# Kernel optimization log

Measured on AMD Instinct MI355X. Metric: run time of the kernel, lower is better.

The kernel has to match this reference:

```python
import jax, jax.numpy as jnp
import numpy as np

H = 3072; NH = 24; HD = 128; MLP_D = 12288
B = 1; IMG = 1536; REF = 512; TXT = 256

def _gelu_tanh(x):
    return jax.nn.gelu(x, approximate=True)

def _ln(x, eps=1e-6):
    m = jnp.mean(x, axis=-1, keepdims=True)
    v = jnp.var(x, axis=-1, keepdims=True)
    return (x - m) * jax.lax.rsqrt(v + eps)

def _rms(x, g, eps=1e-6):
    return x * jax.lax.rsqrt(jnp.mean(x * x, axis=-1, keepdims=True) + eps) * g

def _rot_half(x):
    # interleaved rotate-half: (x0,x1,x2,x3,...) -> (-x1,x0,-x3,x2,...)
    x2 = x.reshape(x.shape[:-1] + (-1, 2))
    return jnp.stack([-x2[..., 1], x2[..., 0]], axis=-1).reshape(x.shape)

def setup_inputs():
    key = jax.random.key(0)
    ks = jax.random.split(key, 16)
    s = 0.02
    # rope tables for image tokens (interleaved layout, values repeated x2)
    inv_freq = 1.0 / (10000.0 ** (jnp.arange(0, HD // 2, dtype=jnp.float32) / (HD // 2)))
    ang = jnp.arange(IMG, dtype=jnp.float32)[:, None] * inv_freq[None, :]   # [IMG, HD//2]
    ang = jnp.repeat(ang, 2, axis=-1)                                       # [IMG, HD]
    return {
        'x':   jax.random.normal(ks[0], (B, IMG + TXT, H), jnp.float32),
        'vec': jax.random.normal(ks[1], (B, H), jnp.float32),
        'ref': jax.random.normal(ks[2], (B, REF, H), jnp.float32),
        'cos': jnp.cos(ang), 'sin': jnp.sin(ang),
        'mod_w':  jax.random.normal(ks[3], (H, 3 * H), jnp.float32) * s,
        'mod_b':  jnp.zeros((3 * H,), jnp.float32),
        'rf1_w':  jax.random.normal(ks[4], (H, H), jnp.float32) * s,
        'rf1_b':  jnp.zeros((H,), jnp.float32),
        'rf2_w':  jax.random.normal(ks[5], (H, H), jnp.float32) * s,
        'rf2_b':  jnp.zeros((H,), jnp.float32),
        'rln_g':  jnp.ones((H,), jnp.float32),
        'rln_b':  jnp.zeros((H,), jnp.float32),
        'lin1_w': jax.random.normal(ks[6], (H, 3 * H + MLP_D), jnp.float32) * s,
        'lin1_b': jnp.zeros((3 * H + MLP_D,), jnp.float32),
        'q_g':    jnp.ones((HD,), jnp.float32),
        'k_g':    jnp.ones((HD,), jnp.float32),
        'lin2_w': jax.random.normal(ks[7], (H + MLP_D, H), jnp.float32) * s,
        'lin2_b': jnp.zeros((H,), jnp.float32),
        'text_mask': jnp.ones((B, TXT), jnp.int32),
        'img_len': IMG, 'txt_len': TXT,
    }

def _forward(x, vec, ref, cos, sin, mod_w, mod_b, rf1_w, rf1_b, rf2_w, rf2_b,
             rln_g, rln_b, lin1_w, lin1_b, q_g, k_g, lin2_w, lin2_b,
             text_mask, img_len, txt_len):
    Bb = x.shape[0]
    ref_len = ref.shape[1]
    # modulation (ModulateDiT: SiLU -> Linear -> chunk(3))
    mod = jnp.dot(jax.nn.silu(vec), mod_w) + mod_b
    shift, scale, gate = jnp.split(mod, 3, axis=-1)
    x_mod = _ln(x) * (1.0 + scale[:, None]) + shift[:, None]
    # ref MLP + affine LayerNorm
    r = jnp.dot(_gelu_tanh(jnp.dot(ref, rf1_w) + rf1_b), rf2_w) + rf2_b
    r = _ln(r) * rln_g + rln_b
    # token reassembly: [img | ref | txt]
    xc = jnp.concatenate([x_mod[:, :img_len], r, x_mod[:, img_len:]], axis=1)
    h = jnp.dot(xc, lin1_w) + lin1_b
    qkv, mlp = h[..., :3 * H], h[..., 3 * H:]
    L2 = xc.shape[1]
    q, k, v = [t.reshape(Bb, L2, NH, HD) for t in jnp.split(qkv, 3, axis=-1)]
    # q drops the ref span; ref contributes K/V only
    q = jnp.concatenate([q[:, :img_len], q[:, img_len + ref_len:]], axis=1)
    q = _rms(q, q_g)
    k = _rms(k, k_g)
    # rotary only on image tokens
    c = cos[None, :, None, :]; s = sin[None, :, None, :]
    img_q = q[:, :img_len] * c + _rot_half(q[:, :img_len]) * s
    img_k = k[:, :img_len] * c + _rot_half(k[:, :img_len]) * s
    q = jnp.concatenate([img_q, q[:, img_len:]], axis=1)          # [B, Lq, NH, HD]
    k = jnp.concatenate([img_k, k[:, img_len:]], axis=1)          # [B, Lkv, NH, HD]
    # varlen mask (cu_seqlens semantics): valid attends valid, pad attends pad
    tmask = text_mask.astype(bool)
    qv  = jnp.concatenate([jnp.ones((Bb, img_len), bool), tmask], axis=1)
    kvv = jnp.concatenate([jnp.ones((Bb, img_len + ref_len), bool), tmask], axis=1)
    allowed = (qv[:, None, :, None] == kvv[:, None, None, :])     # [B,1,Lq,Lkv]
    scores = jnp.einsum('bqhd,bkhd->bhqk', q, k) * (HD ** -0.5)
    scores = jnp.where(allowed, scores, jnp.asarray(-1e9, scores.dtype))
    p = jax.nn.softmax(scores, axis=-1)
    attn = jnp.einsum('bhqk,bkhd->bqhd', p, v).reshape(Bb, img_len + txt_len, H)
    mlp = jnp.concatenate([mlp[:, :img_len], mlp[:, img_len + ref_len:]], axis=1)
    out = jnp.dot(jnp.concatenate([attn, _gelu_tanh(mlp)], axis=-1), lin2_w) + lin2_b
    return x + out * gate[:, None]

def reference(x, vec, ref, cos, sin, mod_w, mod_b, rf1_w, rf1_b, rf2_w, rf2_b,
              rln_g, rln_b, lin1_w, lin1_b, q_g, k_g, lin2_w, lin2_b,
              text_mask, img_len, txt_len):
    return _forward(x, vec, ref, cos, sin, mod_w, mod_b, rf1_w, rf1_b, rf2_w, rf2_b,
                    rln_g, rln_b, lin1_w, lin1_b, q_g, k_g, lin2_w, lin2_b,
                    text_mask, img_len, txt_len)
```

## Files before the change

kernel.cpp:

```cpp
#include <hip/hip_runtime.h>
#include <cstdint>
#include <cstddef>

typedef unsigned short u16;
typedef unsigned int   u32;
typedef __bf16 bf16_t;
typedef bf16_t bf16x8 __attribute__((ext_vector_type(8)));
typedef float  f32x4  __attribute__((ext_vector_type(4)));
typedef u16    u16x4  __attribute__((ext_vector_type(4)));


__device__ __forceinline__ float b2f(u16 b){ u32 u=((u32)b)<<16; float f; __builtin_memcpy(&f,&u,4); return f; }
__device__ __forceinline__ u16 f2b(float f){ u32 u; __builtin_memcpy(&u,&f,4); u = u + 0x7fffu + ((u>>16)&1u); return (u16)(u>>16); }
__device__ __forceinline__ float gelu_f(float x){
  const float u2 = 1.5957691216057308f*(x + 0.044715f*x*x*x);
  return x/(1.f + __expf(-u2));
}

__device__ __forceinline__ void gload_lds16(const void* g, void* l){
  __builtin_amdgcn_global_load_lds((const __attribute__((address_space(1))) void*)g,
                                   (__attribute__((address_space(3))) void*)l, 16, 0, 0);
}

template<int NW, bool MX>
__device__ __forceinline__ float bred(float v, float* red){
  #pragma unroll
  for (int o=32;o;o>>=1){ float u=__shfl_down(v,o,64); v = MX? fmaxf(v,u) : v+u; }
  const int t = threadIdx.x;
  if ((t&63)==0) red[t>>6]=v;
  __syncthreads();
  float r = red[0];
  #pragma unroll
  for (int i=1;i<NW;i++) r = MX? fmaxf(r,red[i]) : r+red[i];
  __syncthreads();
  return r;
}

__device__ __forceinline__ void unpack8(uint4 u, float* f){
  f[0]=b2f((u16)(u.x&0xffffu)); f[1]=b2f((u16)(u.x>>16));
  f[2]=b2f((u16)(u.y&0xffffu)); f[3]=b2f((u16)(u.y>>16));
  f[4]=b2f((u16)(u.z&0xffffu)); f[5]=b2f((u16)(u.z>>16));
  f[6]=b2f((u16)(u.w&0xffffu)); f[7]=b2f((u16)(u.w>>16));
}
__device__ __forceinline__ uint4 pack8(const float* f){
  uint4 u;
  u.x = (u32)f2b(f[0]) | ((u32)f2b(f[1])<<16);
  u.y = (u32)f2b(f[2]) | ((u32)f2b(f[3])<<16);
  u.z = (u32)f2b(f[4]) | ((u32)f2b(f[5])<<16);
  u.w = (u32)f2b(f[6]) | ((u32)f2b(f[7])<<16);
  return u;
}

__global__ void modv_part(const float* __restrict__ vec, const float* __restrict__ W,
                          float* __restrict__ part){
  __shared__ float s[128];
  const int t = threadIdx.x;
  const int j = blockIdx.x*256 + t;
  const int i0 = blockIdx.y*128;
  if (t < 128){ float v = vec[i0+t]; s[t] = v/(1.f+__expf(-v)); }
  __syncthreads();
  float acc = 0.f;
  #pragma unroll 8
  for (int i=0;i<128;i++) acc += s[i]*W[(size_t)(i0+i)*9216 + j];
  part[(size_t)blockIdx.y*9216 + j] = acc;
}
__global__ void modv_reduce(const float* __restrict__ part, const float* __restrict__ mb,
                            float* __restrict__ modp){
  const int j = blockIdx.x*256 + threadIdx.x;
  float a = mb[j];
  #pragma unroll
  for (int c=0;c<24;c++) a += part[(size_t)c*9216 + j];
  modp[j] = a;
}

__global__ __launch_bounds__(256)
void convT(const float* __restrict__ W, u16* __restrict__ Wt, int Kd, int Nd){
  __shared__ float Ls[64][65];
  const int t = threadIdx.x;
  const int n0 = blockIdx.x*64, k0 = blockIdx.y*64;
  const int tr = t>>4;
  const int tc = (t&15)*4;
  #pragma unroll
  for (int p=0;p<4;p++){
    const int kk = tr + p*16;
    const float4 v = *(const float4*)(W + (size_t)(k0+kk)*Nd + n0 + tc);
    Ls[kk][tc+0]=v.x; Ls[kk][tc+1]=v.y; Ls[kk][tc+2]=v.z; Ls[kk][tc+3]=v.w;
  }
  __syncthreads();
  #pragma unroll
  for (int p=0;p<4;p++){
    const int nn = tr + p*16;
    u16x4 o;
    o.x = f2b(Ls[tc+0][nn]); o.y = f2b(Ls[tc+1][nn]);
    o.z = f2b(Ls[tc+2][nn]); o.w = f2b(Ls[tc+3][nn]);
    *(u16x4*)(Wt + (size_t)(n0+nn)*Kd + k0 + tc) = o;
  }
}

__global__ void convertF2B(const float* __restrict__ src, u16* __restrict__ dst){
  const size_t i = ((size_t)blockIdx.x*256 + threadIdx.x)*4;
  const float4 v = *(const float4*)(src+i);
  u16x4 o; o.x=f2b(v.x); o.y=f2b(v.y); o.z=f2b(v.z); o.w=f2b(v.w);
  *(u16x4*)(dst+i) = o;
}

__global__ void ln_modulate(const float* __restrict__ x, const float* __restrict__ modp,
                            u16* __restrict__ xc){
  __shared__ float red[4];
  const int row = blockIdx.x, t = threadIdx.x;
  const float* xr = x + (size_t)row*3072;
  float4 v[3]; float s=0.f, ss=0.f;
  #pragma unroll
  for (int k=0;k<3;k++){
    v[k] = *(const float4*)(xr + t*4 + k*1024);
    s  += v[k].x+v[k].y+v[k].z+v[k].w;
    ss += v[k].x*v[k].x+v[k].y*v[k].y+v[k].z*v[k].z+v[k].w*v[k].w;
  }
  s  = bred<4,false>(s, red);
  ss = bred<4,false>(ss, red);
  const float mean = s*(1.f/3072.f);
  const float inv = rsqrtf(ss*(1.f/3072.f)-mean*mean + 1e-6f);
  const int orow = row<1536 ? row : row+512;
  u16* o = xc + (size_t)orow*3072;
  const float* shiftp = modp; const float* scalep = modp+3072;
  #pragma unroll
  for (int k=0;k<3;k++){
    const int j = t*4 + k*1024;
    const float4 sc = *(const float4*)(scalep+j);
    const float4 sh = *(const float4*)(shiftp+j);
    u16x4 ov;
    ov.x = f2b((v[k].x-mean)*inv*(1.f+sc.x)+sh.x);
    ov.y = f2b((v[k].y-mean)*inv*(1.f+sc.y)+sh.y);
    ov.z = f2b((v[k].z-mean)*inv*(1.f+sc.z)+sh.z);
    ov.w = f2b((v[k].w-mean)*inv*(1.f+sc.w)+sh.w);
    *(u16x4*)(o+j) = ov;
  }
}

__global__ void ln_ref(const float* __restrict__ rt, const float* __restrict__ g,
                       const float* __restrict__ b, u16* __restrict__ xc){
  __shared__ float red[4];
  const int row = blockIdx.x, t = threadIdx.x;
  const float* xr = rt + (size_t)row*3072;
  float4 v[3]; float s=0.f, ss=0.f;
  #pragma unroll
  for (int k=0;k<3;k++){
    v[k] = *(const float4*)(xr + t*4 + k*1024);
    s  += v[k].x+v[k].y+v[k].z+v[k].w;
    ss += v[k].x*v[k].x+v[k].y*v[k].y+v[k].z*v[k].z+v[k].w*v[k].w;
  }
  s  = bred<4,false>(s, red);
  ss = bred<4,false>(ss, red);
  const float mean = s*(1.f/3072.f);
  const float inv = rsqrtf(ss*(1.f/3072.f)-mean*mean + 1e-6f);
  u16* o = xc + (size_t)(1536+row)*3072;
  #pragma unroll
  for (int k=0;k<3;k++){
    const int j = t*4 + k*1024;
    const float4 gv = *(const float4*)(g+j);
    const float4 bv = *(const float4*)(b+j);
    u16x4 ov;
    ov.x = f2b((v[k].x-mean)*inv*gv.x+bv.x);
    ov.y = f2b((v[k].y-mean)*inv*gv.y+bv.y);
    ov.z = f2b((v[k].z-mean)*inv*gv.z+bv.z);
    ov.w = f2b((v[k].w-mean)*inv*gv.w+bv.w);
    *(u16x4*)(o+j) = ov;
  }
}

__global__ void qk_prep(const u16* __restrict__ h, const float* __restrict__ qg,
                        const float* __restrict__ kg, const float* __restrict__ cosb,
                        const float* __restrict__ sinb, u16* __restrict__ Q,
                        u16* __restrict__ Kb){
  __shared__ float red[4];
  const int row = blockIdx.x, hd = blockIdx.y, d = threadIdx.x;
  const u16* hr = h + (size_t)row*21504;
  const float kv = b2f(hr[3072 + hd*128 + d]);
  const bool doq = (row < 1536) || (row >= 2048);
  const float qv = doq ? b2f(hr[hd*128 + d]) : 0.f;
  float a = kv*kv, b = qv*qv;
  #pragma unroll
  for (int o=32;o;o>>=1){ a += __shfl_down(a,o,64); b += __shfl_down(b,o,64); }
  if ((d&63)==0){ red[(d>>6)*2] = a; red[(d>>6)*2+1] = b; }
  __syncthreads();
  const float kinv = rsqrtf((red[0]+red[2])*(1.f/128.f) + 1e-6f);
  const float qinv = rsqrtf((red[1]+red[3])*(1.f/128.f) + 1e-6f);
  float kn = kv*kinv*kg[d];
  float qn = qv*qinv*qg[d];
  if (row < 1536){
    const float c  = cosb[row*128 + d];
    const float sn = sinb[row*128 + d];
    const float ko = b2f(hr[3072 + hd*128 + (d^1)])*kinv*kg[d^1];
    const float qo = b2f(hr[hd*128 + (d^1)])*qinv*qg[d^1];
    const float krh = (d&1) ? ko : -ko;
    const float qrh = (d&1) ? qo : -qo;
    kn = kn*c + krh*sn;
    qn = qn*c + qrh*sn;
  }
  Kb[((size_t)hd*2304 + row)*128 + d] = f2b(kn);
  if (doq){
    const int qrow = row<1536 ? row : row-512;
    Q[((size_t)hd*1792 + qrow)*128 + d] = f2b(qn);
  }
}

__global__ void v_transpose(const u16* __restrict__ h, u16* __restrict__ VT){
  __shared__ u16 Ls[32][33];
  const int tx = threadIdx.x, ty = threadIdx.y;
  const int l0 = blockIdx.x*32, d0 = blockIdx.y*32, hd = blockIdx.z;
  #pragma unroll
  for (int r=0;r<4;r++)
    Ls[ty+r*8][tx] = h[(size_t)(l0+ty+r*8)*21504 + 6144 + hd*128 + d0 + tx];
  __syncthreads();
  #pragma unroll
  for (int r=0;r<4;r++)
    VT[((size_t)hd*128 + d0+ty+r*8)*2304 + l0 + tx] = Ls[tx][ty+r*8];
}

__global__ void gelu_mlp(const u16* __restrict__ h, u16* __restrict__ out2){
  const int q = blockIdx.x;
  const int hrow = q<1536 ? q : q+512;
  const int j = blockIdx.y*2048 + threadIdx.x*8;
  const uint4 u = *(const uint4*)(h + (size_t)hrow*21504 + 9216 + j);
  float f[8]; unpack8(u, f);
  #pragma unroll
  for (int e=0;e<8;e++) f[e] = gelu_f(f[e]);
  const uint4 o = pack8(f);
  *(uint4*)(out2 + (size_t)q*15360 + 3072 + j) = o;
}

template<int EPI>
__global__ __launch_bounds__(256)
void gemm_bt(const u16* __restrict__ A, const u16* __restrict__ Bt,
             const float* __restrict__ bias, void* __restrict__ Cv,
             int K, int ldA, int ldB, int ldC,
             long long sA, long long sB, long long sC)
{
  __shared__ u16 As[128*32];
  __shared__ u16 Bs[128*32];
  const int t = threadIdx.x;
  const int w = t>>6, lane = t&63;
  const int bm = blockIdx.y, bn = blockIdx.x, bz = blockIdx.z;
  const u16* Ab = A + (size_t)((long long)bz*sA) + (size_t)bm*128*ldA;
  const u16* Bb = Bt + (size_t)((long long)bz*sB) + (size_t)bn*128*ldB;
  const int wm = w>>1, wn = w&1;
  const int lr = lane&15, lk = lane>>4;
  const int row0 = t>>2, kp0 = (t&3)*8;
  char* AsB = (char*)As; char* BsB = (char*)Bs;
  const int off0 = w*1024;
  const int off1 = 4096 + w*1024;
  f32x4 acc[4][4] = {};

  for (int kt = 0; kt < K; kt += 32){
    __syncthreads();
    gload_lds16(Ab + (size_t)row0*ldA + kt + kp0,      AsB + off0);
    gload_lds16(Ab + (size_t)(row0+64)*ldA + kt + kp0, AsB + off1);
    gload_lds16(Bb + (size_t)row0*ldB + kt + kp0,      BsB + off0);
    gload_lds16(Bb + (size_t)(row0+64)*ldB + kt + kp0, BsB + off1);
    __syncthreads();
    bf16x8 av[4], bv[4];
    #pragma unroll
    for (int i=0;i<4;i++) av[i] = *(const bf16x8*)(As + (wm*64+i*16+lr)*32 + lk*8);
    #pragma unroll
    for (int j=0;j<4;j++) bv[j] = *(const bf16x8*)(Bs + (wn*64+j*16+lr)*32 + lk*8);
    #pragma unroll
    for (int i=0;i<4;i++)
      #pragma unroll
      for (int j=0;j<4;j++)
        acc[i][j] = __builtin_amdgcn_mfma_f32_16x16x32_bf16(av[i], bv[j], acc[i][j], 0,0,0);
  }

  const int mBase = bm*128 + wm*64;
  const int nBase = bn*128 + wn*64;
  #pragma unroll
  for (int i=0;i<4;i++){
    #pragma unroll
    for (int j=0;j<4;j++){
      #pragma unroll
      for (int r=0;r<4;r++){
        const int m = mBase + i*16 + lk*4 + r;
        const int n = nBase + j*16 + lr;
        const float v = acc[i][j][r];
        const long long idx = (long long)bz*sC + (long long)m*ldC + n;
        if (EPI==6){
          ((float*)Cv)[idx] = v;
        } else {
          ((u16*)Cv)[idx] = f2b(v + bias[n]);
        }
      }
    }
  }
}

__global__ void comb_gelu(const float* __restrict__ P, const float* __restrict__ b,
                          u16* __restrict__ o){
  const size_t e = ((size_t)blockIdx.x*256 + threadIdx.x)*4;
  const int n = (int)(e % 3072);
  const size_t S = (size_t)512*3072;
  float4 a = *(const float4*)(P + e);
  #pragma unroll
  for (int c=1;c<6;c++){
    const float4 p = *(const float4*)(P + c*S + e);
    a.x+=p.x; a.y+=p.y; a.z+=p.z; a.w+=p.w;
  }
  const float4 bb = *(const float4*)(b + n);
  u16x4 ov;
  ov.x = f2b(gelu_f(a.x+bb.x)); ov.y = f2b(gelu_f(a.y+bb.y));
  ov.z = f2b(gelu_f(a.z+bb.z)); ov.w = f2b(gelu_f(a.w+bb.w));
  *(u16x4*)(o + e) = ov;
}
__global__ void comb_bias(const float* __restrict__ P, const float* __restrict__ b,
                          float* __restrict__ o){
  const size_t e = ((size_t)blockIdx.x*256 + threadIdx.x)*4;
  const int n = (int)(e % 3072);
  const size_t S = (size_t)512*3072;
  float4 a = *(const float4*)(P + e);
  #pragma unroll
  for (int c=1;c<6;c++){
    const float4 p = *(const float4*)(P + c*S + e);
    a.x+=p.x; a.y+=p.y; a.z+=p.z; a.w+=p.w;
  }
  const float4 bb = *(const float4*)(b + n);
  float4 ov; ov.x=a.x+bb.x; ov.y=a.y+bb.y; ov.z=a.z+bb.z; ov.w=a.w+bb.w;
  *(float4*)(o + e) = ov;
}

#define G256_BAR()  __builtin_amdgcn_s_barrier()
#define G256_LGKM() do{ asm volatile("s_waitcnt lgkmcnt(0)" ::: "memory"); \
                        __builtin_amdgcn_sched_barrier(0); }while(0)

template<int CEPI>
__global__ __launch_bounds__(512,2)
void gemm256(const u16* __restrict__ A, const u16* __restrict__ Bt,
             const float* __restrict__ bias, void* __restrict__ Cv,
             int Kc, int ld, int ldC, int nbn, int ntile, long long sC, int nwg, int gm)
{
  __shared__ char smem[131072];
  const int t = threadIdx.x;
  const int wid = t>>6, lane = t&63;
  const int lr = lane&15, lk = lane>>4;
  const int wm = wid>>2, wn = wid&3;

  const int orig = blockIdx.x;
  const int q8 = nwg>>3, r8 = nwg&7;
  const int xcd = orig&7, jj = orig>>3;
  const int wg = (xcd<r8 ? xcd*(q8+1) : r8*(q8+1) + (xcd-r8)*q8) + jj;
  int sk, bm, bn;
  if (gm > 0){
    const int band = wg / (gm*nbn);
    const int rr = wg - band*(gm*nbn);
    bn = rr / gm;
    bm = band*gm + (rr - bn*gm);
    sk = 0;
  } else {
    sk = wg / ntile;
    const int rem = wg - sk*ntile;
    bm = rem / nbn; bn = rem % nbn;
  }

  const u16* Agl = A  + (size_t)bm*256*ld + (size_t)sk*Kc;
  const u16* Bgl = Bt + (size_t)bn*256*ld + (size_t)sk*Kc;
  const int NT = Kc>>6;

  const int d0 = wid*64 + lane;
  const int sr = d0>>3;
  const size_t soff = (size_t)sr*ld + (size_t)(((d0&7)^(sr&7))<<3);

  const int xsl0 = ((lk    ) ^ (lr&7))<<4;
  const int xsl1 = ((lk | 4) ^ (lr&7))<<4;

  f32x4 acc[8][4] = {};
  bf16x8 bv[4][2];

  auto STAGE = [&](const u16* g, int h, int kt, char* ldsMat){
    const u16* s0 = g + (size_t)(h*128)*ld + kt + soff;
    char* l0 = ldsMat + h*16384 + wid*1024;
    gload_lds16(s0, l0);
    gload_lds16(s0 + (size_t)64*ld, l0 + 8192);
  };

  STAGE(Agl, 0, 0, smem);
  STAGE(Agl, 1, 0, smem);
  STAGE(Bgl, 0, 0, smem + 32768);
  STAGE(Bgl, 1, 0, smem + 32768);
  if (NT > 1){
    STAGE(Bgl, 0, 64, smem + 65536 + 32768);
    STAGE(Bgl, 1, 64, smem + 65536 + 32768);
    asm volatile("s_waitcnt vmcnt(4)" ::: "memory");
  } else {
    asm volatile("s_waitcnt vmcnt(0)" ::: "memory");
  }
  G256_BAR();

  for (int tt = 0; tt < NT; ++tt){
    char* cA = smem + (tt&1)*65536;
    char* cB = cA + 32768;
    char* nA = smem + ((tt+1)&1)*65536;
    const int kt1 = (tt+1)<<6, kt2 = (tt+2)<<6;
    const bool stA = (tt+1) < NT, stB = (tt+2) < NT;

    {
      const char* ab0 = cA + (wm*128 + 0*32 + lr)*128;
      const char* ab1 = cA + (wm*128 + 1*32 + lr)*128;
      bf16x8 a00 = *(const bf16x8*)(ab0 + xsl0);
      bf16x8 a01 = *(const bf16x8*)(ab0 + xsl1);
      bf16x8 a02 = *(const bf16x8*)(ab0 + 2048 + xsl0);
      bf16x8 a03 = *(const bf16x8*)(ab0 + 2048 + xsl1);
      bf16x8 a10 = *(const bf16x8*)(ab1 + xsl0);
      bf16x8 a11 = *(const bf16x8*)(ab1 + xsl1);
      bf16x8 a12 = *(const bf16x8*)(ab1 + 2048 + xsl0);
      bf16x8 a13 = *(const bf16x8*)(ab1 + 2048 + xsl1);
      #pragma unroll
      for (int j=0;j<4;j++){
        const char* bbase = cB + (wn*64 + j*16 + lr)*128;
        bv[j][0] = *(const bf16x8*)(bbase + xsl0);
        bv[j][1] = *(const bf16x8*)(bbase + xsl1);
      }
      if (stA){ STAGE(Agl, 0, kt1, nA); STAGE(Agl, 1, kt1, nA); }
      G256_BAR();
      G256_LGKM();
      __builtin_amdgcn_s_setprio(1);
      #pragma unroll
      for (int j=0;j<4;j++){
        acc[0][j] = __builtin_amdgcn_mfma_f32_16x16x32_bf16(a00, bv[j][0], acc[0][j], 0,0,0);
        acc[0][j] = __builtin_amdgcn_mfma_f32_16x16x32_bf16(a01, bv[j][1], acc[0][j], 0,0,0);
        acc[1][j] = __builtin_amdgcn_mfma_f32_16x16x32_bf16(a02, bv[j][0], acc[1][j], 0,0,0);
        acc[1][j] = __builtin_amdgcn_mfma_f32_16x16x32_bf16(a03, bv[j][1], acc[1][j], 0,0,0);
        acc[2][j] = __builtin_amdgcn_mfma_f32_16x16x32_bf16(a10, bv[j][0], acc[2][j], 0,0,0);
        acc[2][j] = __builtin_amdgcn_mfma_f32_16x16x32_bf16(a11, bv[j][1], acc[2][j], 0,0,0);
        acc[3][j] = __builtin_amdgcn_mfma_f32_16x16x32_bf16(a12, bv[j][0], acc[3][j], 0,0,0);
        acc[3][j] = __builtin_amdgcn_mfma_f32_16x16x32_bf16(a13, bv[j][1], acc[3][j], 0,0,0);
      }
      __builtin_amdgcn_s_setprio(0);
      G256_BAR();
    }
    {
      const char* ab2 = cA + (wm*128 + 2*32 + lr)*128;
      const char* ab3 = cA + (wm*128 + 3*32 + lr)*128;
      bf16x8 a20 = *(const bf16x8*)(ab2 + xsl0);
      bf16x8 a21 = *(const bf16x8*)(ab2 + xsl1);
      bf16x8 a22 = *(const bf16x8*)(ab2 + 2048 + xsl0);
      bf16x8 a23 = *(const bf16x8*)(ab2 + 2048 + xsl1);
      bf16x8 a30 = *(const bf16x8*)(ab3 + xsl0);
      bf16x8 a31 = *(const bf16x8*)(ab3 + xsl1);
      bf16x8 a32 = *(const bf16x8*)(ab3 + 2048 + xsl0);
      bf16x8 a33 = *(const bf16x8*)(ab3 + 2048 + xsl1);
      if (stB){ STAGE(Bgl, 0, kt2, cB); STAGE(Bgl, 1, kt2, cB); }
      G256_BAR();
      G256_LGKM();
      __builtin_amdgcn_s_setprio(1);
      #pragma unroll
      for (int j=0;j<4;j++){
        acc[4][j] = __builtin_amdgcn_mfma_f32_16x16x32_bf16(a20, bv[j][0], acc[4][j], 0,0,0);
        acc[4][j] = __builtin_amdgcn_mfma_f32_16x16x32_bf16(a21, bv[j][1], acc[4][j], 0,0,0);
        acc[5][j] = __builtin_amdgcn_mfma_f32_16x16x32_bf16(a22, bv[j][0], acc[5][j], 0,0,0);
        acc[5][j] = __builtin_amdgcn_mfma_f32_16x16x32_bf16(a23, bv[j][1], acc[5][j], 0,0,0);
        acc[6][j] = __builtin_amdgcn_mfma_f32_16x16x32_bf16(a30, bv[j][0], acc[6][j], 0,0,0);
        acc[6][j] = __builtin_amdgcn_mfma_f32_16x16x32_bf16(a31, bv[j][1], acc[6][j], 0,0,0);
        acc[7][j] = __builtin_amdgcn_mfma_f32_16x16x32_bf16(a32, bv[j][0], acc[7][j], 0,0,0);
        acc[7][j] = __builtin_amdgcn_mfma_f32_16x16x32_bf16(a33, bv[j][1], acc[7][j], 0,0,0);
      }
      __builtin_amdgcn_s_setprio(0);
      if (stB)      { asm volatile("s_waitcnt vmcnt(4)" ::: "memory"); }
      else if (stA) { asm volatile("s_waitcnt vmcnt(0)" ::: "memory"); }
      G256_BAR();
    }
  }

  const int mB = bm*256 + wm*128 + lk*4;
  const int nB = bn*256 + wn*64 + lr;
  #pragma unroll
  for (int fi=0; fi<8; fi++){
    #pragma unroll
    for (int j=0; j<4; j++){
      const int n = nB + j*16;
      const float bb = (CEPI==0) ? bias[n] : 0.f;
      #pragma unroll
      for (int r=0;r<4;r++){
        const int m = mB + fi*16 + r;
        if (CEPI==0){
          ((u16*)Cv)[(size_t)m*ldC + n] = f2b(acc[fi][j][r] + bb);
        } else {
          ((float*)Cv)[(size_t)sk*sC + (size_t)m*ldC + n] = acc[fi][j][r];
        }
      }
    }
  }
}

__global__ __launch_bounds__(512,4)
void flash_attn(const u16* __restrict__ Qb, const u16* __restrict__ Kb,
                const u16* __restrict__ VT, const int* __restrict__ tmask,
                u16* __restrict__ out2)
{
  __shared__ __attribute__((aligned(16))) char smf[81920];
  char* Ks0 = smf;
  char* Vs0 = smf + 32768;
  char* Ps  = smf + 65536;
  const int t = threadIdx.x, wid = t>>6, lane = t&63;
  const int lr = lane&15, hi = lane>>4;
  const int head = blockIdx.y, qt = blockIdx.x;
  const int q0 = qt*128;
  const u16* Qg = Qb + ((size_t)head*1792 + q0)*128;
  const u16* Kg = Kb + (size_t)head*2304*128;
  const u16* Vg = VT + (size_t)head*128*2304;
  const float SCALE = 0.08838834764831845f;

  u32 kbits = 0;
  #pragma unroll
  for (int i=0;i<16;i++) kbits |= (u32)(tmask[i*16 + lr] != 0) << i;
  int fqr[4];
  #pragma unroll
  for (int r=0;r<4;r++){
    const int q = q0 + wid*16 + hi*4 + r;
    fqr[r] = (q < 1536) ? 1 : (tmask[q-1536] != 0);
  }

  #pragma unroll
  for (int c=0;c<4;c++){
    const int s = c*512 + wid*64 + lane;
    const int row = s>>4, dsl = s&15;
    gload_lds16(Qg + (size_t)row*128 + ((dsl ^ (row&7))<<3),
                Vs0 + (size_t)(c*512 + wid*64)*16);
  }
  #pragma unroll
  for (int c=0;c<2;c++){
    const int s = c*512 + wid*64 + lane;
    const int row = s>>4, dsl = s&15;
    gload_lds16(Kg + (size_t)row*128 + ((dsl ^ (row&7))<<3),
                Ks0 + (size_t)(c*512 + wid*64)*16);
  }
  asm volatile("s_waitcnt vmcnt(0)" ::: "memory");
  __syncthreads();

  bf16x8 av[4];
  {
    const int row = wid*16 + lr;
    #pragma unroll
    for (int ks=0;ks<4;ks++)
      av[ks] = *(const bf16x8*)(Vs0 + row*256 + (((ks*4+hi) ^ (row&7))<<4));
  }
  asm volatile("s_waitcnt lgkmcnt(0)" ::: "memory");
  __builtin_amdgcn_sched_barrier(0);
  __syncthreads();

  #pragma unroll
  for (int c=0;c<2;c++){
    const int s = c*512 + wid*64 + lane;
    const int row = s>>3, dsl = s&7;
    gload_lds16(Vg + (size_t)row*2304 + ((dsl ^ (row&7))<<3),
                Vs0 + (size_t)(c*512 + wid*64)*16);
  }
  asm volatile("s_waitcnt vmcnt(0)" ::: "memory");
  __syncthreads();

  f32x4 acc[8] = {};
  float m_[4], l_[4];
  #pragma unroll
  for (int r=0;r<4;r++){ m_[r] = -3e38f; l_[r] = 0.f; }

  for (int kt = 0; kt < 36; ++kt){
    char* Kc = Ks0 + (kt&1)*16384;
    char* Vc = Vs0 + (kt&1)*16384;
    if (kt+1 < 36){
      char* Kn = Ks0 + ((kt+1)&1)*16384;
      char* Vn = Vs0 + ((kt+1)&1)*16384;
      #pragma unroll
      for (int c=0;c<2;c++){
        const int s = c*512 + wid*64 + lane;
        { const int row = s>>4, dsl = s&15;
          gload_lds16(Kg + (size_t)((kt+1)*64 + row)*128 + ((dsl ^ (row&7))<<3),
                      Kn + (size_t)(c*512 + wid*64)*16); }
        { const int row = s>>3, dsl = s&7;
          gload_lds16(Vg + (size_t)row*2304 + (kt+1)*64 + ((dsl ^ (row&7))<<3),
                      Vn + (size_t)(c*512 + wid*64)*16); }
      }
    }
    f32x4 sacc[4] = {};
    #pragma unroll
    for (int ks=0;ks<4;ks++){
      #pragma unroll
      for (int j=0;j<4;j++){
        const int row = j*16 + lr;
        bf16x8 bk = *(const bf16x8*)(Kc + row*256 + (((ks*4+hi) ^ (row&7))<<4));
        sacc[j] = __builtin_amdgcn_mfma_f32_16x16x32_bf16(av[ks], bk, sacc[j], 0,0,0);
      }
    }
    int gkj[4];
    #pragma unroll
    for (int j=0;j<4;j++)
      gkj[j] = (kt < 32) ? 1 : (int)((kbits >> ((kt-32)*4 + j)) & 1u);
    float p[4][4]; bool alw[4][4];
    float mt[4] = {-3e38f,-3e38f,-3e38f,-3e38f};
    #pragma unroll
    for (int j=0;j<4;j++){
      #pragma unroll
      for (int r=0;r<4;r++){
        const float s = sacc[j][r]*SCALE;
        const bool a = (fqr[r] == gkj[j]);
        alw[j][r] = a; p[j][r] = s;
        if (a) mt[r] = fmaxf(mt[r], s);
      }
    }
    #pragma unroll
    for (int r=0;r<4;r++){
      #pragma unroll
      for (int o=1;o<16;o<<=1) mt[r] = fmaxf(mt[r], __shfl_xor(mt[r], o, 64));
      const float nm = fmaxf(m_[r], mt[r]);
      const float cr = __expf(m_[r] - nm);
      m_[r] = nm;
      l_[r] *= cr;
      #pragma unroll
      for (int jp=0;jp<8;jp++) acc[jp][r] *= cr;
    }
    float rs[4] = {0.f,0.f,0.f,0.f};
    #pragma unroll
    for (int j=0;j<4;j++){
      #pragma unroll
      for (int r=0;r<4;r++){
        const float pv = alw[j][r] ? __expf(p[j][r] - m_[r]) : 0.f;
        p[j][r] = pv; rs[r] += pv;
      }
    }
    #pragma unroll
    for (int r=0;r<4;r++){
      #pragma unroll
      for (int o=1;o<16;o<<=1) rs[r] += __shfl_xor(rs[r], o, 64);
      l_[r] += rs[r];
    }
    #pragma unroll
    for (int j=0;j<4;j++){
      #pragma unroll
      for (int r=0;r<4;r++){
        const int q = wid*16 + hi*4 + r;
        const int k = j*16 + lr;
        *(u16*)(Ps + q*128 + (((k>>3) ^ (q&7))<<4) + (k&7)*2) = f2b(p[j][r]);
      }
    }
    asm volatile("s_waitcnt lgkmcnt(0)" ::: "memory");
    __builtin_amdgcn_sched_barrier(0);
    bf16x8 pa[2];
    {
      const int row = wid*16 + lr;
      #pragma unroll
      for (int ks2=0;ks2<2;ks2++)
        pa[ks2] = *(const bf16x8*)(Ps + row*128 + (((ks2*4+hi) ^ (row&7))<<4));
    }
    #pragma unroll
    for (int ks2=0;ks2<2;ks2++){
      #pragma unroll
      for (int jp=0;jp<8;jp++){
        const int row = jp*16 + lr;
        bf16x8 bvv = *(const bf16x8*)(Vc + row*128 + (((ks2*4+hi) ^ (row&7))<<4));
        acc[jp] = __builtin_amdgcn_mfma_f32_16x16x32_bf16(pa[ks2], bvv, acc[jp], 0,0,0);
      }
    }
    asm volatile("s_waitcnt vmcnt(0)" ::: "memory");
    __syncthreads();
  }

  float inv[4];
  #pragma unroll
  for (int r=0;r<4;r++) inv[r] = 1.f/l_[r];
  #pragma unroll
  for (int jp=0;jp<8;jp++){
    #pragma unroll
    for (int r=0;r<4;r++){
      const size_t q = q0 + wid*16 + hi*4 + r;
      out2[q*15360 + head*128 + jp*16 + lr] = f2b(acc[jp][r]*inv[r]);
    }
  }
}

__global__ void lin2_fin(const float* __restrict__ P, const float* __restrict__ x,
                         const float* __restrict__ bias, const float* __restrict__ gate,
                         float* __restrict__ out){
  const size_t e = ((size_t)blockIdx.x*256 + threadIdx.x)*4;
  const int n = (int)(e % 3072);
  const size_t S = (size_t)1792*3072;
  float4 a = *(const float4*)(P + e);
  #pragma unroll
  for (int c=1;c<6;c++){
    const float4 p = *(const float4*)(P + c*S + e);
    a.x+=p.x; a.y+=p.y; a.z+=p.z; a.w+=p.w;
  }
  const float4 bb = *(const float4*)(bias + n);
  const float4 gg = *(const float4*)(gate + n);
  const float4 xv = *(const float4*)(x + e);
  float4 o;
  o.x = xv.x + (a.x+bb.x)*gg.x;
  o.y = xv.y + (a.y+bb.y)*gg.y;
  o.z = xv.z + (a.z+bb.z)*gg.z;
  o.w = xv.w + (a.w+bb.w)*gg.w;
  *(float4*)(out + e) = o;
}

extern "C" void kernel_launch(void* const* d_in, const int* in_sizes, int n_in,
                              void* d_out, int out_size, void* d_ws, size_t ws_size,
                              hipStream_t stream)
{
  (void)in_sizes; (void)n_in; (void)out_size; (void)ws_size;
  const float* x     = (const float*)d_in[0];
  const float* vec   = (const float*)d_in[1];
  const float* ref   = (const float*)d_in[2];
  const float* cosb  = (const float*)d_in[3];
  const float* sinb  = (const float*)d_in[4];
  const float* mod_w = (const float*)d_in[5];
  const float* mod_b = (const float*)d_in[6];
  const float* rf1_w = (const float*)d_in[7];
  const float* rf1_b = (const float*)d_in[8];
  const float* rf2_w = (const float*)d_in[9];
  const float* rf2_b = (const float*)d_in[10];
  const float* rln_g = (const float*)d_in[11];
  const float* rln_b = (const float*)d_in[12];
  const float* lin1_w= (const float*)d_in[13];
  const float* lin1_b= (const float*)d_in[14];
  const float* q_g   = (const float*)d_in[15];
  const float* k_g   = (const float*)d_in[16];
  const float* lin2_w= (const float*)d_in[17];
  const float* lin2_b= (const float*)d_in[18];
  const int*   tmask = (const int*)d_in[19];
  float* out = (float*)d_out;
  char* ws = (char*)d_ws;

  float* modp = (float*)(ws + 0);
  float* part = (float*)(ws + 36864);
  u16*  w2t   = (u16*)(ws + 921600);
  u16*  Qb    = (u16*)(ws + 95293440ll);
  u16*  Kb    = (u16*)(ws + 106303488ll);
  u16*  VT    = (u16*)(ws + 120459264ll);
  u16*  out2  = (u16*)(ws + 134615040ll);
  u16*  w1t   = (u16*)(ws + 189665280ll);
  u16*  xc    = (u16*)(ws + 321785856ll);
  u16*  rf1t  = (u16*)(ws + 335941632ll);
  u16*  rf2t  = (u16*)(ws + 354816000ll);
  u16*  refb  = (u16*)(ws + 373690368ll);
  u16*  tb    = (u16*)(ws + 376836096ll);
  float* rtmp = (float*)(ws + 379981824ll);
  float* rp   = (float*)(ws + 386273280ll);
  u16*  hbuf  = (u16*)(ws + 335941632ll);
  float* p2b  = (float*)(ws + 189665280ll);

  modv_part<<<dim3(36,24),256,0,stream>>>(vec, mod_w, part);
  modv_reduce<<<36,256,0,stream>>>(part, mod_b, modp);
  convT<<<dim3(48,48),  256,0,stream>>>(rf1_w, rf1t, 3072, 3072);
  convT<<<dim3(48,48),  256,0,stream>>>(rf2_w, rf2t, 3072, 3072);
  convT<<<dim3(336,48), 256,0,stream>>>(lin1_w, w1t, 3072, 21504);
  convT<<<dim3(48,240), 256,0,stream>>>(lin2_w, w2t, 15360, 3072);
  convertF2B<<<1536,256,0,stream>>>(ref, refb);
  ln_modulate<<<1792,256,0,stream>>>(x, modp, xc);
  gemm_bt<6><<<dim3(24,4,6),256,0,stream>>>(refb, rf1t, nullptr, rp, 512, 3072,3072,3072,
                                            512,512, (long long)512*3072);
  comb_gelu<<<1536,256,0,stream>>>(rp, rf1_b, tb);
  gemm_bt<6><<<dim3(24,4,6),256,0,stream>>>(tb, rf2t, nullptr, rp, 512, 3072,3072,3072,
                                            512,512, (long long)512*3072);
  comb_bias<<<1536,256,0,stream>>>(rp, rf2_b, rtmp);
  ln_ref<<<512,256,0,stream>>>(rtmp, rln_g, rln_b, xc);
  gemm256<0><<<756,512,0,stream>>>(xc, w1t, lin1_b, hbuf, 3072, 3072, 21504, 84, 756, 0, 756, 3);
  gelu_mlp<<<dim3(1792,6),256,0,stream>>>(hbuf, out2);
  qk_prep<<<dim3(2304,24),128,0,stream>>>(hbuf, q_g, k_g, cosb, sinb, Qb, Kb);
  v_transpose<<<dim3(72,4,24),dim3(32,8),0,stream>>>(hbuf, VT);
  flash_attn<<<dim3(14,24),512,0,stream>>>(Qb, Kb, VT, tmask, out2);
  gemm256<1><<<504,512,0,stream>>>(out2, w2t, nullptr, p2b, 2560, 15360, 3072, 12, 84,
                                   (long long)1792*3072, 504, 0);
  lin2_fin<<<5376,256,0,stream>>>(p2b, x, lin2_b, modp + 6144, out);
}
```

Baseline: 906.6 us.

## Skip unused lin1 tiles for ref tokens and make the GEMM persistent

Result: no change. 905.7 us (-0.1%).

```diff
diff --git a/kernel.cpp b/kernel.cpp
--- a/kernel.cpp
+++ b/kernel.cpp
@@ -329,6 +329,18 @@
 #define G256_LGKM() do{ asm volatile("s_waitcnt lgkmcnt(0)" ::: "memory"); \
                         __builtin_amdgcn_sched_barrier(0); }while(0)
 
+__device__ __forceinline__ void lin1_map(int tw, int& bm, int& bn){
+  if (tw < 504){
+    const int band = tw/252; const int rr = tw - band*252;
+    bn = rr/3; bm = band*3 + (rr - bn*3);
+  } else if (tw < 588){
+    bm = 8; bn = tw - 504;
+  } else {
+    const int rem = tw - 588;
+    bm = 6 + (rem&1); bn = 12 + (rem>>1);
+  }
+}
+
 template<int CEPI>
 __global__ __launch_bounds__(512,2)
 void gemm256(const u16* __restrict__ A, const u16* __restrict__ Bt,
@@ -341,150 +353,160 @@
   const int lr = lane&15, lk = lane>>4;
   const int wm = wid>>2, wn = wid&3;
 
-  const int orig = blockIdx.x;
-  const int q8 = nwg>>3, r8 = nwg&7;
-  const int xcd = orig&7, jj = orig>>3;
-  const int wg = (xcd<r8 ? xcd*(q8+1) : r8*(q8+1) + (xcd-r8)*q8) + jj;
-  int sk, bm, bn;
-  if (gm > 0){
-    const int band = wg / (gm*nbn);
-    const int rr = wg - band*(gm*nbn);
-    bn = rr / gm;
-    bm = band*gm + (rr - bn*gm);
-    sk = 0;
+  int niter = 1;
+  int bmA[2], bnA[2], skA[2];
+  if (gm == -1){
+    const int b = blockIdx.x;
+    lin1_map(b, bmA[0], bnA[0]); skA[0] = 0;
+    if (b + 512 < 636){ lin1_map(b + 512, bmA[1], bnA[1]); skA[1] = 0; niter = 2; }
   } else {
-    sk = wg / ntile;
-    const int rem = wg - sk*ntile;
-    bm = rem / nbn; bn = rem % nbn;
-  }
-
-  const u16* Agl = A  + (size_t)bm*256*ld + (size_t)sk*Kc;
-  const u16* Bgl = Bt + (size_t)bn*256*ld + (size_t)sk*Kc;
+    const int orig = blockIdx.x;
+    const int q8 = nwg>>3, r8 = nwg&7;
+    const int xcd = orig&7, jj = orig>>3;
+    const int wg = (xcd<r8 ? xcd*(q8+1) : r8*(q8+1) + (xcd-r8)*q8) + jj;
+    if (gm > 0){
+      const int band = wg / (gm*nbn);
+      const int rr = wg - band*(gm*nbn);
+      bnA[0] = rr / gm;
+      bmA[0] = band*gm + (rr - bnA[0]*gm);
+      skA[0] = 0;
+    } else {
+      skA[0] = wg / ntile;
+      const int rem = wg - skA[0]*ntile;
+      bmA[0] = rem / nbn; bnA[0] = rem % nbn;
+    }
+  }
+
   const int NT = Kc>>6;
-
   const int d0 = wid*64 + lane;
   const int sr = d0>>3;
   const size_t soff = (size_t)sr*ld + (size_t)(((d0&7)^(sr&7))<<3);
-
   const int xsl0 = ((lk    ) ^ (lr&7))<<4;
   const int xsl1 = ((lk | 4) ^ (lr&7))<<4;
 
-  f32x4 acc[8][4] = {};
-  bf16x8 bv[4][2];
-
-  auto STAGE = [&](const u16* g, int h, int kt, char* ldsMat){
-    const u16* s0 = g + (size_t)(h*128)*ld + kt + soff;
-    char* l0 = ldsMat + h*16384 + wid*1024;
-    gload_lds16(s0, l0);
-    gload_lds16(s0 + (size_t)64*ld, l0 + 8192);
-  };
-
-  STAGE(Agl, 0, 0, smem);
-  STAGE(Agl, 1, 0, smem);
-  STAGE(Bgl, 0, 0, smem + 32768);
-  STAGE(Bgl, 1, 0, smem + 32768);
-  if (NT > 1){
-    STAGE(Bgl, 0, 64, smem + 65536 + 32768);
-    STAGE(Bgl, 1, 64, smem + 65536 + 32768);
-    asm volatile("s_waitcnt vmcnt(4)" ::: "memory");
-  } else {
-    asm volatile("s_waitcnt vmcnt(0)" ::: "memory");
-  }
-  G256_BAR();
-
-  for (int tt = 0; tt < NT; ++tt){
-    char* cA = smem + (tt&1)*65536;
-    char* cB = cA + 32768;
-    char* nA = smem + ((tt+1)&1)*65536;
-    const int kt1 = (tt+1)<<6, kt2 = (tt+2)<<6;
-    const bool stA = (tt+1) < NT, stB = (tt+2) < NT;
-
-    {
-      const char* ab0 = cA + (wm*128 + 0*32 + lr)*128;
-      const char* ab1 = cA + (wm*128 + 1*32 + lr)*128;
-      bf16x8 a00 = *(const bf16x8*)(ab0 + xsl0);
-      bf16x8 a01 = *(const bf16x8*)(ab0 + xsl1);
-      bf16x8 a02 = *(const bf16x8*)(ab0 + 2048 + xsl0);
-      bf16x8 a03 = *(const bf16x8*)(ab0 + 2048 + xsl1);
-      bf16x8 a10 = *(const bf16x8*)(ab1 + xsl0);
-      bf16x8 a11 = *(const bf16x8*)(ab1 + xsl1);
-      bf16x8 a12 = *(const bf16x8*)(ab1 + 2048 + xsl0);
-      bf16x8 a13 = *(const bf16x8*)(ab1 + 2048 + xsl1);
-      #pragma unroll
-      for (int j=0;j<4;j++){
-        const char* bbase = cB + (wn*64 + j*16 + lr)*128;
-        bv[j][0] = *(const bf16x8*)(bbase + xsl0);
-        bv[j][1] = *(const bf16x8*)(bbase + xsl1);
-      }
-      if (stA){ STAGE(Agl, 0, kt1, nA); STAGE(Agl, 1, kt1, nA); }
-      G256_BAR();
-      G256_LGKM();
-      __builtin_amdgcn_s_setprio(1);
-      #pragma unroll
-      for (int j=0;j<4;j++){
-        acc[0][j] = __builtin_amdgcn_mfma_f32_16x16x32_bf16(a00, bv[j][0], acc[0][j], 0,0,0);
-        acc[0][j] = __builtin_amdgcn_mfma_f32_16x16x32_bf16(a01, bv[j][1], acc[0][j], 0,0,0);
-        acc[1][j] = __builtin_amdgcn_mfma_f32_16x16x32_bf16(a02, bv[j][0], acc[1][j], 0,0,0);
-        acc[1][j] = __builtin_amdgcn_mfma_f32_16x16x32_bf16(a03, bv[j][1], acc[1][j], 0,0,0);
-        acc[2][j] = __builtin_amdgcn_mfma_f32_16x16x32_bf16(a10, bv[j][0], acc[2][j], 0,0,0);
-        acc[2][j] = __builtin_amdgcn_mfma_f32_16x16x32_bf16(a11, bv[j][1], acc[2][j], 0,0,0);
-        acc[3][j] = __builtin_amdgcn_mfma_f32_16x16x32_bf16(a12, bv[j][0], acc[3][j], 0,0,0);
-        acc[3][j] = __builtin_amdgcn_mfma_f32_16x16x32_bf16(a13, bv[j][1], acc[3][j], 0,0,0);
-      }
-      __builtin_amdgcn_s_setprio(0);
-      G256_BAR();
-    }
-    {
-      const char* ab2 = cA + (wm*128 + 2*32 + lr)*128;
-      const char* ab3 = cA + (wm*128 + 3*32 + lr)*128;
-      bf16x8 a20 = *(const bf16x8*)(ab2 + xsl0);
-      bf16x8 a21 = *(const bf16x8*)(ab2 + xsl1);
-      bf16x8 a22 = *(const bf16x8*)(ab2 + 2048 + xsl0);
-      bf16x8 a23 = *(const bf16x8*)(ab2 + 2048 + xsl1);
-      bf16x8 a30 = *(const bf16x8*)(ab3 + xsl0);
-      bf16x8 a31 = *(const bf16x8*)(ab3 + xsl1);
-      bf16x8 a32 = *(const bf16x8*)(ab3 + 2048 + xsl0);
-      bf16x8 a33 = *(const bf16x8*)(ab3 + 2048 + xsl1);
-      if (stB){ STAGE(Bgl, 0, kt2, cB); STAGE(Bgl, 1, kt2, cB); }
-      G256_BAR();
-      G256_LGKM();
-      __builtin_amdgcn_s_setprio(1);
-      #pragma unroll
-      for (int j=0;j<4;j++){
-        acc[4][j] = __builtin_amdgcn_mfma_f32_16x16x32_bf16(a20, bv[j][0], acc[4][j], 0,0,0);
-        acc[4][j] = __builtin_amdgcn_mfma_f32_16x16x32_bf16(a21, bv[j][1], acc[4][j], 0,0,0);
-        acc[5][j] = __builtin_amdgcn_mfma_f32_16x16x32_bf16(a22, bv[j][0], acc[5][j], 0,0,0);
-        acc[5][j] = __builtin_amdgcn_mfma_f32_16x16x32_bf16(a23, bv[j][1], acc[5][j], 0,0,0);
-        acc[6][j] = __builtin_amdgcn_mfma_f32_16x16x32_bf16(a30, bv[j][0], acc[6][j], 0,0,0);
-        acc[6][j] = __builtin_amdgcn_mfma_f32_16x16x32_bf16(a31, bv[j][1], acc[6][j], 0,0,0);
-        acc[7][j] = __builtin_amdgcn_mfma_f32_16x16x32_bf16(a32, bv[j][0], acc[7][j], 0,0,0);
-        acc[7][j] = __builtin_amdgcn_mfma_f32_16x16x32_bf16(a33, bv[j][1], acc[7][j], 0,0,0);
-      }
-      __builtin_amdgcn_s_setprio(0);
-      if (stB)      { asm volatile("s_waitcnt vmcnt(4)" ::: "memory"); }
-      else if (stA) { asm volatile("s_waitcnt vmcnt(0)" ::: "memory"); }
-      G256_BAR();
-    }
-  }
-
-  const int mB = bm*256 + wm*128 + lk*4;
-  const int nB = bn*256 + wn*64 + lr;
-  #pragma unroll
-  for (int fi=0; fi<8; fi++){
-    #pragma unroll
-    for (int j=0; j<4; j++){
-      const int n = nB + j*16;
-      const float bb = (CEPI==0) ? bias[n] : 0.f;
-      #pragma unroll
-      for (int r=0;r<4;r++){
-        const int m = mB + fi*16 + r;
-        if (CEPI==0){
-          ((u16*)Cv)[(size_t)m*ldC + n] = f2b(acc[fi][j][r] + bb);
-        } else {
-          ((float*)Cv)[(size_t)sk*sC + (size_t)m*ldC + n] = acc[fi][j][r];
+  for (int it = 0; it < niter; ++it){
+    const int bm = bmA[it], bn = bnA[it], sk = skA[it];
+    const u16* Agl = A  + (size_t)bm*256*ld + (size_t)sk*Kc;
+    const u16* Bgl = Bt + (size_t)bn*256*ld + (size_t)sk*Kc;
+
+    f32x4 acc[8][4] = {};
+    bf16x8 bv[4][2];
+
+    auto STAGE = [&](const u16* g, int h, int kt, char* ldsMat){
+      const u16* s0 = g + (size_t)(h*128)*ld + kt + soff;
+      char* l0 = ldsMat + h*16384 + wid*1024;
+      gload_lds16(s0, l0);
+      gload_lds16(s0 + (size_t)64*ld, l0 + 8192);
+    };
+
+    STAGE(Agl, 0, 0, smem);
+    STAGE(Agl, 1, 0, smem);
+    STAGE(Bgl, 0, 0, smem + 32768);
+    STAGE(Bgl, 1, 0, smem + 32768);
+    if (NT > 1){
+      STAGE(Bgl, 0, 64, smem + 65536 + 32768);
+      STAGE(Bgl, 1, 64, smem + 65536 + 32768);
+      asm volatile("s_waitcnt vmcnt(4)" ::: "memory");
+    } else {
+      asm volatile("s_waitcnt vmcnt(0)" ::: "memory");
+    }
+    G256_BAR();
+
+    for (int tt = 0; tt < NT; ++tt){
+      char* cA = smem + (tt&1)*65536;
+      char* cB = cA + 32768;
+      char* nA = smem + ((tt+1)&1)*65536;
+      const int kt1 = (tt+1)<<6, kt2 = (tt+2)<<6;
+      const bool stA = (tt+1) < NT, stB = (tt+2) < NT;
+
+      {
+        const char* ab0 = cA + (wm*128 + 0*32 + lr)*128;
+        const char* ab1 = cA + (wm*128 + 1*32 + lr)*128;
+        bf16x8 a00 = *(const bf16x8*)(ab0 + xsl0);
+        bf16x8 a01 = *(const bf16x8*)(ab0 + xsl1);
+        bf16x8 a02 = *(const bf16x8*)(ab0 + 2048 + xsl0);
+        bf16x8 a03 = *(const bf16x8*)(ab0 + 2048 + xsl1);
+        bf16x8 a10 = *(const bf16x8*)(ab1 + xsl0);
+        bf16x8 a11 = *(const bf16x8*)(ab1 + xsl1);
+        bf16x8 a12 = *(const bf16x8*)(ab1 + 2048 + xsl0);
+        bf16x8 a13 = *(const bf16x8*)(ab1 + 2048 + xsl1);
+        #pragma unroll
+        for (int j=0;j<4;j++){
+          const char* bbase = cB + (wn*64 + j*16 + lr)*128;
+          bv[j][0] = *(const bf16x8*)(bbase + xsl0);
+          bv[j][1] = *(const bf16x8*)(bbase + xsl1);
         }
-      }
-    }
+        if (stA){ STAGE(Agl, 0, kt1, nA); STAGE(Agl, 1, kt1, nA); }
+        G256_BAR();
+        G256_LGKM();
+        __builtin_amdgcn_s_setprio(1);
+        #pragma unroll
+        for (int j=0;j<4;j++){
+          acc[0][j] = __builtin_amdgcn_mfma_f32_16x16x32_bf16(a00, bv[j][0], acc[0][j], 0,0,0);
+          acc[0][j] = __builtin_amdgcn_mfma_f32_16x16x32_bf16(a01, bv[j][1], acc[0][j], 0,0,0);
+          acc[1][j] = __builtin_amdgcn_mfma_f32_16x16x32_bf16(a02, bv[j][0], acc[1][j], 0,0,0);
+          acc[1][j] = __builtin_amdgcn_mfma_f32_16x16x32_bf16(a03, bv[j][1], acc[1][j], 0,0,0);
+          acc[2][j] = __builtin_amdgcn_mfma_f32_16x16x32_bf16(a10, bv[j][0], acc[2][j], 0,0,0);
+          acc[2][j] = __builtin_amdgcn_mfma_f32_16x16x32_bf16(a11, bv[j][1], acc[2][j], 0,0,0);
+          acc[3][j] = __builtin_amdgcn_mfma_f32_16x16x32_bf16(a12, bv[j][0], acc[3][j], 0,0,0);
+          acc[3][j] = __builtin_amdgcn_mfma_f32_16x16x32_bf16(a13, bv[j][1], acc[3][j], 0,0,0);
+        }
+        __builtin_amdgcn_s_setprio(0);
+        G256_BAR();
+      }
+      {
+        const char* ab2 = cA + (wm*128 + 2*32 + lr)*128;
+        const char* ab3 = cA + (wm*128 + 3*32 + lr)*128;
+        bf16x8 a20 = *(const bf16x8*)(ab2 + xsl0);
+        bf16x8 a21 = *(const bf16x8*)(ab2 + xsl1);
+        bf16x8 a22 = *(const bf16x8*)(ab2 + 2048 + xsl0);
+        bf16x8 a23 = *(const bf16x8*)(ab2 + 2048 + xsl1);
+        bf16x8 a30 = *(const bf16x8*)(ab3 + xsl0);
+        bf16x8 a31 = *(const bf16x8*)(ab3 + xsl1);
+        bf16x8 a32 = *(const bf16x8*)(ab3 + 2048 + xsl0);
+        bf16x8 a33 = *(const bf16x8*)(ab3 + 2048 + xsl1);
+        if (stB){ STAGE(Bgl, 0, kt2, cB); STAGE(Bgl, 1, kt2, cB); }
+        G256_BAR();
+        G256_LGKM();
+        __builtin_amdgcn_s_setprio(1);
+        #pragma unroll
+        for (int j=0;j<4;j++){
+          acc[4][j] = __builtin_amdgcn_mfma_f32_16x16x32_bf16(a20, bv[j][0], acc[4][j], 0,0,0);
+          acc[4][j] = __builtin_amdgcn_mfma_f32_16x16x32_bf16(a21, bv[j][1], acc[4][j], 0,0,0);
+          acc[5][j] = __builtin_amdgcn_mfma_f32_16x16x32_bf16(a22, bv[j][0], acc[5][j], 0,0,0);
+          acc[5][j] = __builtin_amdgcn_mfma_f32_16x16x32_bf16(a23, bv[j][1], acc[5][j], 0,0,0);
+          acc[6][j] = __builtin_amdgcn_mfma_f32_16x16x32_bf16(a30, bv[j][0], acc[6][j], 0,0,0);
+          acc[6][j] = __builtin_amdgcn_mfma_f32_16x16x32_bf16(a31, bv[j][1], acc[6][j], 0,0,0);
+          acc[7][j] = __builtin_amdgcn_mfma_f32_16x16x32_bf16(a32, bv[j][0], acc[7][j], 0,0,0);
+          acc[7][j] = __builtin_amdgcn_mfma_f32_16x16x32_bf16(a33, bv[j][1], acc[7][j], 0,0,0);
+        }
+        __builtin_amdgcn_s_setprio(0);
+        if (stB)      { asm volatile("s_waitcnt vmcnt(4)" ::: "memory"); }
+        else if (stA) { asm volatile("s_waitcnt vmcnt(0)" ::: "memory"); }
+        G256_BAR();
+      }
+    }
+
+    const int mB = bm*256 + wm*128 + lk*4;
+    const int nB = bn*256 + wn*64 + lr;
+    #pragma unroll
+    for (int fi=0; fi<8; fi++){
+      #pragma unroll
+      for (int j=0; j<4; j++){
+        const int n = nB + j*16;
+        const float bb = (CEPI==0) ? bias[n] : 0.f;
+        #pragma unroll
+        for (int r=0;r<4;r++){
+          const int m = mB + fi*16 + r;
+          if (CEPI==0){
+            ((u16*)Cv)[(size_t)m*ldC + n] = f2b(acc[fi][j][r] + bb);
+          } else {
+            ((float*)Cv)[(size_t)sk*sC + (size_t)m*ldC + n] = acc[fi][j][r];
+          }
+        }
+      }
+    }
+    if (it+1 < niter) __syncthreads();
   }
 }
 
@@ -756,7 +778,7 @@
                                             512,512, (long long)512*3072);
   comb_bias<<<1536,256,0,stream>>>(rp, rf2_b, rtmp);
   ln_ref<<<512,256,0,stream>>>(rtmp, rln_g, rln_b, xc);
-  gemm256<0><<<756,512,0,stream>>>(xc, w1t, lin1_b, hbuf, 3072, 3072, 21504, 84, 756, 0, 756, 3);
+  gemm256<0><<<512,512,0,stream>>>(xc, w1t, lin1_b, hbuf, 3072, 3072, 21504, 84, 636, 0, 512, -1);
   gelu_mlp<<<dim3(1792,6),256,0,stream>>>(hbuf, out2);
   qk_prep<<<dim3(2304,24),128,0,stream>>>(hbuf, q_g, k_g, cosb, sinb, Qb, Kb);
   v_transpose<<<dim3(72,4,24),dim3(32,8),0,stream>>>(hbuf, VT);
```
